# Kernel optimization log

Measured on AMD Instinct MI355X. Metric: run time of the kernel, lower is better.

## Reference

```python
import jax, jax.numpy as jnp
import numpy as np

T, B, D_IN, H = 512, 128, 1024, 2048

def _lstm_cell(x, h, c, W_ih, W_hh, b):
    # PyTorch LSTMCell gate order: i, f, g, o
    gates = x @ W_ih.T + h @ W_hh.T + b  # [B, 4H]
    i, f, g, o = jnp.split(gates, 4, axis=-1)
    c_new = jax.nn.sigmoid(f) * c + jax.nn.sigmoid(i) * jnp.tanh(g)
    h_new = jax.nn.sigmoid(o) * jnp.tanh(c_new)
    return h_new, c_new

def setup_inputs() -> dict:
    key = jax.random.key(0)
    ks = jax.random.split(key, 12)
    k = 1.0 / np.sqrt(H)  # torch LSTMCell init range
    u = lambda kk, shape: jax.random.uniform(kk, shape, jnp.float32, -k, k)
    return {
        "input_seq": jax.random.normal(ks[0], (T, B, D_IN), jnp.float32),
        "h0": jax.random.normal(ks[1], (2, B, H), jnp.float32),
        "c0": jax.random.normal(ks[2], (2, B, H), jnp.float32),
        "W_ih0": u(ks[3], (4 * H, D_IN)),
        "W_hh0": u(ks[4], (4 * H, H)),
        "b0": u(ks[5], (4 * H,)),
        "W_ih1": u(ks[6], (4 * H, H)),
        "W_hh1": u(ks[7], (4 * H, H)),
        "b1": u(ks[8], (4 * H,)),
    }

def reference(input_seq, h0, c0, W_ih0, W_hh0, b0, W_ih1, W_hh1, b1):
    def step(carry, x_t):
        h0_, c0_, h1_, c1_ = carry
        h0n, c0n = _lstm_cell(x_t, h0_, c0_, W_ih0, W_hh0, b0)
        h1n, c1n = _lstm_cell(h0n, h1_, c1_, W_ih1, W_hh1, b1)
        return (h0n, c0n, h1n, c1n), None

    init = (h0[0], c0[0], h0[1], c0[1])
    (h0f, c0f, h1f, c1f), _ = jax.lax.scan(step, init, input_seq)
    return h1f  # last layer hidden at final timestep [B, H]
```

## Files before the change

kernel.cpp:

```cpp
#include <hip/hip_runtime.h>
#include <stdint.h>
#include <stddef.h>

#define T_STEPS 512
#define B_SZ    128
#define DIN     1024
#define H_SZ    2048
#define NG      8192
#define BH      (B_SZ * H_SZ)

typedef __attribute__((ext_vector_type(8))) short bf16x8;
typedef __attribute__((ext_vector_type(4))) float f32x4;

static __device__ __forceinline__ unsigned short f2bf(float x) {
  unsigned int u = __float_as_uint(x);
  u += 0x7fffu + ((u >> 16) & 1u);
  return (unsigned short)(u >> 16);
}

static __device__ __forceinline__ float sigm(float x) {
  return 1.0f / (1.0f + __expf(-x));
}
static __device__ __forceinline__ float tanh_(float x) {
  float e = __expf(-2.0f * fabsf(x));
  float t = (1.0f - e) / (1.0f + e);
  return x < 0.0f ? -t : t;
}

static __device__ __forceinline__ void async_load16(const void* gsrc, void* ldst) {
  __builtin_amdgcn_global_load_lds(
      (__attribute__((address_space(1))) void*)(const_cast<void*>(gsrc)),
      (__attribute__((address_space(3))) void*)ldst,
      16, 0, 0);
}

static __device__ __forceinline__ void wg_barrier_pinned() {
  __builtin_amdgcn_s_barrier();
  asm volatile("" ::: "memory");
  __builtin_amdgcn_sched_barrier(0);
}

__global__ void cvt_x_bf16(const float4* __restrict__ in, ushort4* __restrict__ out, int n4) {
  int i = blockIdx.x * blockDim.x + threadIdx.x;
  int st = gridDim.x * blockDim.x;
  for (; i < n4; i += st) {
    float4 v = in[i];
    ushort4 o;
    o.x = f2bf(v.x); o.y = f2bf(v.y); o.z = f2bf(v.z); o.w = f2bf(v.w);
    out[i] = o;
  }
}

__global__ void build_wcat(const float* __restrict__ wa, const float* __restrict__ wb,
                           unsigned short* __restrict__ outw, int ka, int K) {
  int k = blockIdx.x * blockDim.x + threadIdx.x;
  int n = blockIdx.y;
  if (k >= K) return;
  int kb = K - ka;
  float v = (k < ka) ? wa[(size_t)n * ka + k]
                     : wb[(size_t)n * kb + (k - ka)];
  outw[(size_t)n * K + k] = f2bf(v);
}

__global__ void init_state(const float* __restrict__ h0, const float* __restrict__ c0,
                           unsigned short* __restrict__ hb0, unsigned short* __restrict__ hb1,
                           float* __restrict__ cws) {
  int i = blockIdx.x * blockDim.x + threadIdx.x;
  if (i < BH) {
    hb0[i] = f2bf(h0[i]);
    hb1[i] = f2bf(h0[BH + i]);
    cws[i] = c0[i];
    cws[BH + i] = c0[BH + i];
  }
}

template<int K, int KSPLIT>
static __device__ __forceinline__ void lstm_step_body(
    unsigned short (*Bbuf)[128 * 64],
    const unsigned short* __restrict__ a0,
    const unsigned short* __restrict__ a1,
    const unsigned short* __restrict__ w,
    const float* __restrict__ bias,
    float* __restrict__ c,
    unsigned short* __restrict__ hout,
    float* __restrict__ fout,
    int tid, int lane, int wv, int mb, int n0h)
{
  constexpr int KT = K >> 6;
  f32x4 acc[8] = {};

  const int arow = mb * 64 + wv * 16 + (lane & 15);
  const unsigned short* r0p = a0 + (size_t)arow * KSPLIT;
  const unsigned short* r1p = a1 + (size_t)arow * H_SZ;
  const int klo = (lane >> 4) << 3;

  auto loadA = [&](int kt, bf16x8 (&A)[2]) {
    const int kb = kt << 6;
    const bool sA = kb < KSPLIT;
    const unsigned short* bp = (sA ? r0p : r1p) + (sA ? kb : kb - KSPLIT) + klo;
    A[0] = *(const bf16x8*)(bp);
    A[1] = *(const bf16x8*)(bp + 32);
  };

  auto stageB = [&](int kt) {
    const int kb = kt << 6;
#pragma unroll
    for (int it = 0; it < 4; ++it) {
      int cid = it * 256 + tid;
      int nl  = cid >> 3;
      int chs = (cid & 7) ^ (nl & 7);
      int nn  = ((nl >> 5) << 11) + n0h + (nl & 31);
      const unsigned short* src = w + (size_t)nn * K + kb + (chs << 3);
      async_load16(src, &Bbuf[kt & 3][(it * 256 + wv * 64) * 8]);
    }
  };

  auto iter = [&](int kt, bf16x8 (&A)[2]) {
    if (kt + 3 < KT) stageB(kt + 3);
    const int bq = kt & 3;
#pragma unroll
    for (int kkk = 0; kkk < 2; ++kkk) {
      const int ch = kkk * 4 + (lane >> 4);
      const int cswz = (ch ^ (lane & 7)) << 3;
      bf16x8 bfr[8];
#pragma unroll
      for (int ct = 0; ct < 8; ++ct)
        bfr[ct] = *(const bf16x8*)&Bbuf[bq][(ct * 16 + (lane & 15)) * 64 + cswz];
#pragma unroll
      for (int ct = 0; ct < 8; ++ct)
        acc[ct] = __builtin_amdgcn_mfma_f32_16x16x32_bf16(A[kkk], bfr[ct], acc[ct], 0, 0, 0);
    }
    if (kt + 4 < KT) loadA(kt + 4, A);
    int rem = KT - 1 - kt;
    if (rem >= 4)      asm volatile("s_waitcnt vmcnt(14)" ::: "memory");
    else if (rem == 3) asm volatile("s_waitcnt vmcnt(12)" ::: "memory");
    else if (rem == 2) asm volatile("s_waitcnt vmcnt(6)"  ::: "memory");
    else if (rem == 1) asm volatile("s_waitcnt vmcnt(0)"  ::: "memory");
    wg_barrier_pinned();
  };

  asm volatile("s_waitcnt vmcnt(0)" ::: "memory");

  bf16x8 A0[2], A1[2], A2[2], A3[2];
  stageB(0); loadA(0, A0);
  stageB(1); loadA(1, A1);
  stageB(2); loadA(2, A2);
  loadA(3, A3);
  asm volatile("s_waitcnt vmcnt(16)" ::: "memory");
  wg_barrier_pinned();

  for (int kt = 0; kt < KT; kt += 4) {
    iter(kt,     A0);
    iter(kt + 1, A1);
    iter(kt + 2, A2);
    iter(kt + 3, A3);
  }

#pragma unroll
  for (int p = 0; p < 2; ++p) {
    const int hc = n0h + p * 16 + (lane & 15);
    const float bi  = bias[hc];
    const float bff = bias[H_SZ + hc];
    const float bg  = bias[2 * H_SZ + hc];
    const float bo  = bias[3 * H_SZ + hc];
#pragma unroll
    for (int r = 0; r < 4; ++r) {
      int row = mb * 64 + wv * 16 + ((lane >> 4) << 2) + r;
      size_t idx = (size_t)row * H_SZ + hc;
      float iv = sigm(acc[p    ][r] + bi);
      float fv = sigm(acc[p + 2][r] + bff);
      float gv = tanh_(acc[p + 4][r] + bg);
      float ov = sigm(acc[p + 6][r] + bo);
      float cn = fv * c[idx] + iv * gv;
      c[idx] = cn;
      float hn = ov * tanh_(cn);
      hout[idx] = f2bf(hn);
      if (fout) fout[idx] = hn;
    }
  }
}

template<int K, int KSPLIT>
__global__ __launch_bounds__(256) void lstm_one(
    const unsigned short* __restrict__ a0, const unsigned short* __restrict__ a1,
    const unsigned short* __restrict__ w,  const float* __restrict__ bias,
    float* __restrict__ c, unsigned short* __restrict__ hout, float* __restrict__ fout)
{
  __shared__ __align__(16) unsigned short Bbuf[4][128 * 64];
  const int tid = threadIdx.x, lane = tid & 63, wv = tid >> 6;
  const int mb = blockIdx.x >> 6, n0h = (blockIdx.x & 63) << 5;
  lstm_step_body<K, KSPLIT>(Bbuf, a0, a1, w, bias, c, hout, fout, tid, lane, wv, mb, n0h);
}

template<int K1, int KS1, int K2, int KS2>
__global__ __launch_bounds__(256) void lstm_pair(
    const unsigned short* __restrict__ a0_1, const unsigned short* __restrict__ a1_1,
    const unsigned short* __restrict__ w1,   const float* __restrict__ bias1,
    float* __restrict__ c1, unsigned short* __restrict__ h1out,
    const unsigned short* __restrict__ a0_2, const unsigned short* __restrict__ a1_2,
    const unsigned short* __restrict__ w2,   const float* __restrict__ bias2,
    float* __restrict__ c2, unsigned short* __restrict__ h2out)
{
  __shared__ __align__(16) unsigned short Bbuf[4][128 * 64];
  const int tid = threadIdx.x, lane = tid & 63, wv = tid >> 6;
  if (blockIdx.x < 128) {
    const int mb = blockIdx.x >> 6, n0h = (blockIdx.x & 63) << 5;
    lstm_step_body<K1, KS1>(Bbuf, a0_1, a1_1, w1, bias1, c1, h1out, nullptr, tid, lane, wv, mb, n0h);
  } else {
    const int W = blockIdx.x - 128;
    const int mb = W >> 6, n0h = (W & 63) << 5;
    lstm_step_body<K2, KS2>(Bbuf, a0_2, a1_2, w2, bias2, c2, h2out, nullptr, tid, lane, wv, mb, n0h);
  }
}

extern "C" void kernel_launch(void* const* d_in, const int* in_sizes, int n_in,
                              void* d_out, int out_size, void* d_ws, size_t ws_size,
                              hipStream_t stream) {
  (void)in_sizes; (void)n_in; (void)out_size; (void)ws_size;
  const float* x    = (const float*)d_in[0];
  const float* h0   = (const float*)d_in[1];
  const float* c0   = (const float*)d_in[2];
  const float* Wih0 = (const float*)d_in[3];
  const float* Whh0 = (const float*)d_in[4];
  const float* b0   = (const float*)d_in[5];
  const float* Wih1 = (const float*)d_in[6];
  const float* Whh1 = (const float*)d_in[7];
  const float* b1   = (const float*)d_in[8];
  float* out = (float*)d_out;

  unsigned short* xbf = (unsigned short*)d_ws;
  unsigned short* Wc0 = xbf + (size_t)T_STEPS * B_SZ * DIN;
  unsigned short* Wc1 = Wc0 + (size_t)NG * 3072;
  unsigned short* hb0 = Wc1 + (size_t)NG * 4096;
  unsigned short* hb1 = hb0 + 2 * (size_t)BH;
  float*          cws = (float*)(hb1 + 2 * (size_t)BH);

  cvt_x_bf16<<<dim3(4096), dim3(256), 0, stream>>>(
      (const float4*)x, (ushort4*)xbf, T_STEPS * B_SZ * DIN / 4);
  build_wcat<<<dim3(12, NG), dim3(256), 0, stream>>>(Wih0, Whh0, Wc0, DIN, 3072);
  build_wcat<<<dim3(16, NG), dim3(256), 0, stream>>>(Wih1, Whh1, Wc1, H_SZ, 4096);
  init_state<<<dim3(BH / 256), dim3(256), 0, stream>>>(h0, c0, hb0, hb1, cws);

  lstm_one<3072, 1024><<<dim3(128), dim3(256), 0, stream>>>(
      xbf, hb0 + 0, Wc0, b0, cws, hb0 + BH, nullptr);

  for (int t = 0; t < T_STEPS - 1; ++t) {
    const unsigned short* h0cur = hb0 + (size_t)((t + 1) & 1) * BH;
    lstm_pair<4096, 2048, 3072, 1024><<<dim3(256), dim3(256), 0, stream>>>(
           h0cur, hb1 + (size_t)(t & 1) * BH, Wc1, b1,
                    cws + BH, hb1 + (size_t)((t + 1) & 1) * BH,
         xbf + (size_t)(t + 1) * B_SZ * DIN, h0cur, Wc0, b0,
                    cws, hb0 + (size_t)(t & 1) * BH);
  }
  lstm_one<4096, 2048><<<dim3(128), dim3(256), 0, stream>>>(
      hb0 + 0, hb1 + BH, Wc1, b1, cws + BH, hb1 + 0, out);
}
```

Baseline: 19.93 ms.

## Fuse 16 LSTM timesteps per launch with per-row flag-based inter-block sync

```diff
diff --git a/kernel.cpp b/kernel.cpp
--- a/kernel.cpp
+++ b/kernel.cpp
@@ -38,6 +38,14 @@
   __builtin_amdgcn_s_barrier();
   asm volatile("" ::: "memory");
   __builtin_amdgcn_sched_barrier(0);
+}
+
+static __device__ __forceinline__ void publish(unsigned* flag, unsigned v) {
+  __syncthreads();
+  if (threadIdx.x == 0) {
+    __threadfence();
+    __hip_atomic_store(flag, v, __ATOMIC_RELEASE, __HIP_MEMORY_SCOPE_AGENT);
+  }
 }
 
 __global__ void cvt_x_bf16(const float4* __restrict__ in, ushort4* __restrict__ out, int n4) {
@@ -64,8 +72,9 @@
 
 __global__ void init_state(const float* __restrict__ h0, const float* __restrict__ c0,
                            unsigned short* __restrict__ hb0, unsigned short* __restrict__ hb1,
-                           float* __restrict__ cws) {
+                           float* __restrict__ cws, unsigned* __restrict__ flags) {
   int i = blockIdx.x * blockDim.x + threadIdx.x;
+  if (i < 4096) flags[i] = 0u;
   if (i < BH) {
     hb0[i] = f2bf(h0[i]);
     hb1[i] = f2bf(h0[BH + i]);
@@ -184,32 +193,62 @@
 __global__ __launch_bounds__(256) void lstm_one(
     const unsigned short* __restrict__ a0, const unsigned short* __restrict__ a1,
     const unsigned short* __restrict__ w,  const float* __restrict__ bias,
-    float* __restrict__ c, unsigned short* __restrict__ hout, float* __restrict__ fout)
+    float* __restrict__ c, unsigned short* __restrict__ hout, float* __restrict__ fout,
+    unsigned* __restrict__ postbase)
 {
   __shared__ __align__(16) unsigned short Bbuf[4][128 * 64];
   const int tid = threadIdx.x, lane = tid & 63, wv = tid >> 6;
   const int mb = blockIdx.x >> 6, n0h = (blockIdx.x & 63) << 5;
   lstm_step_body<K, KSPLIT>(Bbuf, a0, a1, w, bias, c, hout, fout, tid, lane, wv, mb, n0h);
-}
-
-template<int K1, int KS1, int K2, int KS2>
-__global__ __launch_bounds__(256) void lstm_pair(
-    const unsigned short* __restrict__ a0_1, const unsigned short* __restrict__ a1_1,
-    const unsigned short* __restrict__ w1,   const float* __restrict__ bias1,
-    float* __restrict__ c1, unsigned short* __restrict__ h1out,
-    const unsigned short* __restrict__ a0_2, const unsigned short* __restrict__ a1_2,
-    const unsigned short* __restrict__ w2,   const float* __restrict__ bias2,
-    float* __restrict__ c2, unsigned short* __restrict__ h2out)
+  if (postbase) publish(postbase + blockIdx.x * 16, 1u);
+}
+
+__global__ __launch_bounds__(256) void lstm_fusedG(
+    const unsigned short* __restrict__ xbf,
+    const unsigned short* __restrict__ Wc1, const float* __restrict__ b1,
+    const unsigned short* __restrict__ Wc0, const float* __restrict__ b0,
+    unsigned short* __restrict__ hb0, unsigned short* __restrict__ hb1,
+    float* __restrict__ c1buf, float* __restrict__ c0buf,
+    unsigned* __restrict__ flg, int tbase, int G)
 {
   __shared__ __align__(16) unsigned short Bbuf[4][128 * 64];
   const int tid = threadIdx.x, lane = tid & 63, wv = tid >> 6;
-  if (blockIdx.x < 128) {
-    const int mb = blockIdx.x >> 6, n0h = (blockIdx.x & 63) << 5;
-    lstm_step_body<K1, KS1>(Bbuf, a0_1, a1_1, w1, bias1, c1, h1out, nullptr, tid, lane, wv, mb, n0h);
-  } else {
-    const int W = blockIdx.x - 128;
-    const int mb = W >> 6, n0h = (W & 63) << 5;
-    lstm_step_body<K2, KS2>(Bbuf, a0_2, a1_2, w2, bias2, c2, h2out, nullptr, tid, lane, wv, mb, n0h);
+  const bool isL1 = blockIdx.x < 128;
+  const int W = isL1 ? blockIdx.x : blockIdx.x - 128;
+  const int mb = W >> 6, n0h = (W & 63) << 5;
+  unsigned* f0 = flg;
+  unsigned* f1 = flg + 2048;
+  unsigned* myflag = (isL1 ? f1 : f0) + W * 16;
+
+  for (int g = 0; g < G; ++g) {
+    const int t = tbase + g;
+    if (tid < 64) {
+      const unsigned* f = f0 + (mb * 64 + tid) * 16;
+      while (__hip_atomic_load(f, __ATOMIC_ACQUIRE, __HIP_MEMORY_SCOPE_AGENT)
+             < (unsigned)(t + 1))
+        __builtin_amdgcn_s_sleep(16);
+    } else if (tid < 128) {
+      const unsigned* f = f1 + (mb * 64 + (tid - 64)) * 16;
+      while (__hip_atomic_load(f, __ATOMIC_ACQUIRE, __HIP_MEMORY_SCOPE_AGENT)
+             < (unsigned)t)
+        __builtin_amdgcn_s_sleep(16);
+    }
+    __syncthreads();
+
+    const unsigned short* h0cur = hb0 + (size_t)((t + 1) & 1) * BH;
+    if (isL1) {
+      lstm_step_body<4096, 2048>(Bbuf, h0cur, hb1 + (size_t)(t & 1) * BH,
+                                 Wc1, b1, c1buf,
+                                 hb1 + (size_t)((t + 1) & 1) * BH, nullptr,
+                                 tid, lane, wv, mb, n0h);
+      publish(myflag, (unsigned)(t + 1));
+    } else {
+      lstm_step_body<3072, 1024>(Bbuf, xbf + (size_t)(t + 1) * B_SZ * DIN, h0cur,
+                                 Wc0, b0, c0buf,
+                                 hb0 + (size_t)(t & 1) * BH, nullptr,
+                                 tid, lane, wv, mb, n0h);
+      publish(myflag, (unsigned)(t + 2));
+    }
   }
 }
 
@@ -234,24 +273,25 @@
   unsigned short* hb0 = Wc1 + (size_t)NG * 4096;
   unsigned short* hb1 = hb0 + 2 * (size_t)BH;
   float*          cws = (float*)(hb1 + 2 * (size_t)BH);
+  unsigned*       flg = (unsigned*)(cws + 2 * (size_t)BH);
 
   cvt_x_bf16<<<dim3(4096), dim3(256), 0, stream>>>(
       (const float4*)x, (ushort4*)xbf, T_STEPS * B_SZ * DIN / 4);
   build_wcat<<<dim3(12, NG), dim3(256), 0, stream>>>(Wih0, Whh0, Wc0, DIN, 3072);
   build_wcat<<<dim3(16, NG), dim3(256), 0, stream>>>(Wih1, Whh1, Wc1, H_SZ, 4096);
-  init_state<<<dim3(BH / 256), dim3(256), 0, stream>>>(h0, c0, hb0, hb1, cws);
+  init_state<<<dim3(BH / 256), dim3(256), 0, stream>>>(h0, c0, hb0, hb1, cws, flg);
 
   lstm_one<3072, 1024><<<dim3(128), dim3(256), 0, stream>>>(
-      xbf, hb0 + 0, Wc0, b0, cws, hb0 + BH, nullptr);
-
-  for (int t = 0; t < T_STEPS - 1; ++t) {
-    const unsigned short* h0cur = hb0 + (size_t)((t + 1) & 1) * BH;
-    lstm_pair<4096, 2048, 3072, 1024><<<dim3(256), dim3(256), 0, stream>>>(
-           h0cur, hb1 + (size_t)(t & 1) * BH, Wc1, b1,
-                    cws + BH, hb1 + (size_t)((t + 1) & 1) * BH,
-         xbf + (size_t)(t + 1) * B_SZ * DIN, h0cur, Wc0, b0,
-                    cws, hb0 + (size_t)(t & 1) * BH);
-  }
+      xbf, hb0 + 0, Wc0, b0, cws, hb0 + BH, nullptr, flg);
+
+  int t = 0;
+  while (t < T_STEPS - 1) {
+    int G = (T_STEPS - 1 - t < 16) ? (T_STEPS - 1 - t) : 16;
+    lstm_fusedG<<<dim3(256), dim3(256), 0, stream>>>(
+        xbf, Wc1, b1, Wc0, b0, hb0, hb1, cws + BH, cws, flg, t, G);
+    t += G;
+  }
+
   lstm_one<4096, 2048><<<dim3(128), dim3(256), 0, stream>>>(
-      hb0 + 0, hb1 + BH, Wc1, b1, cws + BH, hb1 + 0, out);
-}
+      hb0 + 0, hb1 + BH, Wc1, b1, cws + BH, hb1 + 0, out, nullptr);
+}
```

Result: slower. 38.15 ms (+91.4%).
